# Kernel tuning notes

Measured on AMD Instinct MI355X. Metric: run time of the kernel, lower is better.

## Reference

```python
import jax, jax.numpy as jnp
import numpy as np

H = 8        # num_heads
D = 768      # d_model
DH = D // H  # d_head = 96


def setup_inputs() -> dict:
    key = jax.random.key(0)
    ks = jax.random.split(key, 12)
    B, S = 4, 2048
    s_in = 1.0 / np.sqrt(D)
    s_cat = 1.0 / np.sqrt(D)
    return {
        "input_querys": jax.random.normal(ks[0], (B, S, D), jnp.float32),
        "input_key": jax.random.normal(ks[1], (B, S, D), jnp.float32),
        "input_values": jax.random.normal(ks[2], (B, S, D), jnp.float32),
        # per-head projection weights, stacked over the head axis
        "Wq": jax.random.normal(ks[3], (H, D, DH), jnp.float32) * s_in,
        "bq": jax.random.normal(ks[4], (H, DH), jnp.float32) * s_in,
        "Wk": jax.random.normal(ks[5], (H, D, DH), jnp.float32) * s_in,
        "bk": jax.random.normal(ks[6], (H, DH), jnp.float32) * s_in,
        "Wv": jax.random.normal(ks[7], (H, D, DH), jnp.float32) * s_in,
        "bv": jax.random.normal(ks[8], (H, DH), jnp.float32) * s_in,
        # output linear: (H*DH) -> D
        "Wo": jax.random.normal(ks[9], (H * DH, D), jnp.float32) * s_cat,
        "bo": jax.random.normal(ks[10], (D,), jnp.float32) * s_cat,
    }


def reference(input_querys, input_key, input_values, Wq, bq, Wk, bk, Wv, bv, Wo, bo):
    # Per-head linear projections (vectorized over the head axis)
    # q/k/v: [B,S,D] -> [B,H,S,DH]
    Q = jnp.einsum("bsd,hdk->bhsk", input_querys, Wq) + bq[None, :, None, :]
    K = jnp.einsum("bsd,hdk->bhsk", input_key, Wk) + bk[None, :, None, :]
    V = jnp.einsum("bsd,hdk->bhsk", input_values, Wv) + bv[None, :, None, :]

    scale = 1.0 / jnp.sqrt(jnp.asarray(DH, Q.dtype))
    scores = jnp.einsum("bhsk,bhtk->bhst", Q, K) * scale  # [B,H,S,S]
    attn = jax.nn.softmax(scores, axis=-1)
    out = jnp.einsum("bhst,bhtk->bhsk", attn, V)  # [B,H,S,DH]

    # concat heads (head-major order matches torch.cat over ModuleList)
    B, _, S, _ = out.shape
    cat = out.transpose(0, 2, 1, 3).reshape(B, S, H * DH)
    return cat @ Wo + bo
```

## Files before the change

### kernel.cpp

```cpp
#include <hip/hip_runtime.h>


typedef unsigned short u16;
typedef _Float16 h16;
typedef h16 h16x8 __attribute__((ext_vector_type(8)));
typedef __fp16 fp16x2 __attribute__((ext_vector_type(2)));
typedef __fp16 fp16x4 __attribute__((ext_vector_type(4)));
typedef unsigned short u16x8 __attribute__((ext_vector_type(8)));
typedef unsigned short u16x4 __attribute__((ext_vector_type(4)));
typedef float f32x4 __attribute__((ext_vector_type(4)));

__device__ __forceinline__ u16 f2h(float f) {
  union { h16 h; u16 u; } c; c.h = (h16)f; return c.u;
}

__device__ __forceinline__ void gll16(const void* g, void* l) {
  __builtin_amdgcn_global_load_lds(
      (const __attribute__((address_space(1))) void*)g,
      (__attribute__((address_space(3))) void*)l, 16, 0, 0);
}

__global__ __launch_bounds__(256) void prep_kernel(
    const float* __restrict__ Wq, const float* __restrict__ Wk,
    const float* __restrict__ Wv, const float* __restrict__ Wo,
    const float* __restrict__ Xk, const float* __restrict__ Xv,
    const float* __restrict__ Xq,
    u16* __restrict__ WqT, u16* __restrict__ WkT,
    u16* __restrict__ WvT, u16* __restrict__ WoT,
    u16* __restrict__ Xk16, u16* __restrict__ Xv16, u16* __restrict__ Xq16)
{
  const int bid = blockIdx.x;
  const int tid = threadIdx.x;

  if (bid >= 432) {
    const int i = bid - 432;
    const int t = i / 3072;
    const long e = ((long)(i % 3072) * 256 + tid) * 8;
    const float* src = (t == 0) ? Xk : (t == 1) ? Xv : Xq;
    u16* dst = (t == 0) ? Xk16 : (t == 1) ? Xv16 : Xq16;
    f32x4 a = *(const f32x4*)(&src[e]);
    f32x4 b = *(const f32x4*)(&src[e + 4]);
    u16x8 v;
    #pragma unroll
    for (int j = 0; j < 4; j++) { v[j] = f2h(a[j]); v[4 + j] = f2h(b[j]); }
    *(u16x8*)(&dst[e]) = v;
    return;
  }

  if (bid < 288) {
    __shared__ u16 Lt[96][72];
    const int w = bid / 96;
    const int r = bid % 96;
    const int h = r / 12, dt = r % 12;
    const float* W = (w == 0) ? Wq : (w == 1) ? Wk : Wv;
    u16* T = (w == 0) ? WqT : (w == 1) ? WkT : WvT;
    const float* src = W + (size_t)h * 73728 + (size_t)dt * 64 * 96;
    #pragma unroll
    for (int p = 0; p < 6; p++) {
      const int lin = p * 1024 + tid * 4;
      f32x4 v = *(const f32x4*)(&src[lin]);
      const int d = lin / 96, kk = lin % 96;
      #pragma unroll
      for (int j = 0; j < 4; j++) Lt[kk + j][d] = f2h(v[j]);
    }
    __syncthreads();
    #pragma unroll
    for (int c = 0; c < 3; c++) {
      const int ch = c * 256 + tid;
      const int kk = ch >> 3, dc = ch & 7;
      u16x8 o = *(const u16x8*)(&Lt[kk][dc * 8]);
      *(u16x8*)(&T[(size_t)(h * 96 + kk) * 768 + dt * 64 + dc * 8]) = o;
    }
    return;
  }

  {
    __shared__ u16 Lo[64][72];
    const int i = bid - 288;
    const int kt = i / 12, nt = i % 12;
    const float* src = Wo + (size_t)(kt * 64) * 768 + nt * 64;
    #pragma unroll
    for (int p = 0; p < 4; p++) {
      const int lin = p * 1024 + tid * 4;
      const int kr = lin >> 6, nc = lin & 63;
      f32x4 v = *(const f32x4*)(&src[(size_t)kr * 768 + nc]);
      #pragma unroll
      for (int j = 0; j < 4; j++) Lo[nc + j][kr] = f2h(v[j]);
    }
    __syncthreads();
    #pragma unroll
    for (int c = 0; c < 2; c++) {
      const int ch = c * 256 + tid;
      const int nr = ch >> 3, kc = ch & 7;
      u16x8 o = *(const u16x8*)(&Lo[nr][kc * 8]);
      *(u16x8*)(&WoT[(size_t)(nt * 64 + nr) * 768 + kt * 64 + kc * 8]) = o;
    }
  }
}

#define GK 768

__global__ __launch_bounds__(256) void gemm_qkv(
    const u16* __restrict__ Xq16, const u16* __restrict__ Xk16,
    const u16* __restrict__ Xv16, const u16* __restrict__ WT,
    const float* __restrict__ bq, const float* __restrict__ bk,
    const float* __restrict__ bv,
    u16* __restrict__ Q16, u16* __restrict__ K16, u16* __restrict__ VT)
{
  const int z = blockIdx.z;
  const u16* BT = WT + (size_t)z * 589824;
  const float* bias = (z == 0) ? bq : (z == 1) ? bk : bv;
  const u16* A = (z == 0) ? Xq16 : (z == 1) ? Xk16 : Xv16;

  __shared__ __align__(16) u16 Sb[16384];

  const int tid = threadIdx.x;
  const int wave = tid >> 6;
  const int lane = tid & 63;
  const int quad = lane >> 4;
  const int l16 = lane & 15;
  const int m0 = blockIdx.x * 128;
  const int n0 = blockIdx.y * 128;

  f32x4 acc[2][8];
  #pragma unroll
  for (int i = 0; i < 2; i++)
    #pragma unroll
    for (int j = 0; j < 8; j++) acc[i][j] = (f32x4){0.f, 0.f, 0.f, 0.f};

  const int c0 = tid, c1 = tid + 256;
  const u16* gA0 = A + (size_t)(m0 + (c0 >> 2)) * GK + (c0 & 3) * 8;
  const u16* gA1 = A + (size_t)(m0 + (c1 >> 2)) * GK + (c1 & 3) * 8;
  const u16* gB0 = BT + (size_t)(n0 + (c0 >> 2)) * GK + (c0 & 3) * 8;
  const u16* gB1 = BT + (size_t)(n0 + (c1 >> 2)) * GK + (c1 & 3) * 8;
  const int ld0 = (wave * 64) * 8;
  const int ld1 = (256 + wave * 64) * 8;

#define STAGE(buf, kt) do {                                        \
    const int k0_ = (kt) * 32;                                     \
    u16* dst_ = Sb + (buf) * 8192;                                 \
    gll16(gA0 + k0_, dst_ + ld0);                                  \
    gll16(gA1 + k0_, dst_ + ld1);                                  \
    gll16(gB0 + k0_, dst_ + 4096 + ld0);                           \
    gll16(gB1 + k0_, dst_ + 4096 + ld1);                           \
  } while (0)

  STAGE(0, 0);
  int buf = 0;
  for (int kt = 0; kt < 24; kt++) {
    if (kt + 1 < 24) {
      STAGE(buf ^ 1, kt + 1);
      asm volatile("s_waitcnt vmcnt(4)" ::: "memory");
    } else {
      asm volatile("s_waitcnt vmcnt(0)" ::: "memory");
    }
    __builtin_amdgcn_s_barrier();

    const u16* As = Sb + buf * 8192;
    const u16* Bs = As + 4096;
    h16x8 af[2], bf[8];
    #pragma unroll
    for (int mf = 0; mf < 2; mf++)
      af[mf] = *(const h16x8*)(&As[(wave * 32 + mf * 16 + l16) * 32 + quad * 8]);
    #pragma unroll
    for (int nf = 0; nf < 8; nf++)
      bf[nf] = *(const h16x8*)(&Bs[(nf * 16 + l16) * 32 + quad * 8]);
    #pragma unroll
    for (int mf = 0; mf < 2; mf++)
      #pragma unroll
      for (int nf = 0; nf < 8; nf++)
        acc[mf][nf] = __builtin_amdgcn_mfma_f32_16x16x32_f16(af[mf], bf[nf], acc[mf][nf], 0, 0, 0);

    __builtin_amdgcn_s_barrier();
    buf ^= 1;
  }
#undef STAGE

  if (z == 2) {
    const int b = m0 >> 11, s0 = m0 & 2047;
    u16* Ts = Sb;
    #pragma unroll
    for (int half = 0; half < 2; half++) {
      __syncthreads();
      #pragma unroll
      for (int nf2 = 0; nf2 < 4; nf2++) {
        const int nf = half * 4 + nf2;
        const float bv2 = bias[n0 + nf * 16 + l16];
        #pragma unroll
        for (int mf = 0; mf < 2; mf++)
          #pragma unroll
          for (int r = 0; r < 4; r++)
            Ts[(nf2 * 16 + l16) * 136 + wave * 32 + mf * 16 + quad * 4 + r] =
                f2h(acc[mf][nf][r] + bv2);
      }
      __syncthreads();
      #pragma unroll
      for (int p = 0; p < 4; p++) {
        const int c = p * 256 + tid;
        const int row = c >> 4, col8 = (c & 15) * 8;
        u16x8 o8 = *(const u16x8*)(&Ts[row * 136 + col8]);
        *(u16x8*)(&VT[(size_t)b * 768 * 2048 +
                      (size_t)(n0 + half * 64 + row) * 2048 + s0 + col8]) = o8;
      }
    }
    return;
  }

  u16* Yr = (z == 0) ? Q16 : K16;
  #pragma unroll
  for (int nf = 0; nf < 8; nf++) {
    const int n = n0 + nf * 16 + l16;
    const float bv2 = bias[n];
    #pragma unroll
    for (int mf = 0; mf < 2; mf++) {
      const int m = m0 + wave * 32 + mf * 16 + quad * 4;
      #pragma unroll
      for (int r = 0; r < 4; r++)
        Yr[(size_t)(m + r) * GK + n] = f2h(acc[mf][nf][r] + bv2);
    }
  }
}

__global__ __launch_bounds__(256) void gemm_o(
    const u16* __restrict__ A, const u16* __restrict__ BT,
    const float* __restrict__ bias, float* __restrict__ Y)
{
  __shared__ __align__(16) u16 Sb[16384];

  const int tid = threadIdx.x;
  const int wave = tid >> 6;
  const int lane = tid & 63;
  const int quad = lane >> 4;
  const int l16 = lane & 15;
  const int m0 = blockIdx.x * 128;
  const int n0 = blockIdx.y * 128;

  f32x4 acc[2][8];
  #pragma unroll
  for (int i = 0; i < 2; i++)
    #pragma unroll
    for (int j = 0; j < 8; j++) acc[i][j] = (f32x4){0.f, 0.f, 0.f, 0.f};

  const int c0 = tid, c1 = tid + 256;
  const u16* gA0 = A + (size_t)(m0 + (c0 >> 2)) * GK + (c0 & 3) * 8;
  const u16* gA1 = A + (size_t)(m0 + (c1 >> 2)) * GK + (c1 & 3) * 8;
  const u16* gB0 = BT + (size_t)(n0 + (c0 >> 2)) * GK + (c0 & 3) * 8;
  const u16* gB1 = BT + (size_t)(n0 + (c1 >> 2)) * GK + (c1 & 3) * 8;
  const int ld0 = (wave * 64) * 8;
  const int ld1 = (256 + wave * 64) * 8;

#define STAGE(buf, kt) do {                                        \
    const int k0_ = (kt) * 32;                                     \
    u16* dst_ = Sb + (buf) * 8192;                                 \
    gll16(gA0 + k0_, dst_ + ld0);                                  \
    gll16(gA1 + k0_, dst_ + ld1);                                  \
    gll16(gB0 + k0_, dst_ + 4096 + ld0);                           \
    gll16(gB1 + k0_, dst_ + 4096 + ld1);                           \
  } while (0)

  STAGE(0, 0);
  int buf = 0;
  for (int kt = 0; kt < 24; kt++) {
    if (kt + 1 < 24) {
      STAGE(buf ^ 1, kt + 1);
      asm volatile("s_waitcnt vmcnt(4)" ::: "memory");
    } else {
      asm volatile("s_waitcnt vmcnt(0)" ::: "memory");
    }
    __builtin_amdgcn_s_barrier();

    const u16* As = Sb + buf * 8192;
    const u16* Bs = As + 4096;
    h16x8 af[2], bf[8];
    #pragma unroll
    for (int mf = 0; mf < 2; mf++)
      af[mf] = *(const h16x8*)(&As[(wave * 32 + mf * 16 + l16) * 32 + quad * 8]);
    #pragma unroll
    for (int nf = 0; nf < 8; nf++)
      bf[nf] = *(const h16x8*)(&Bs[(nf * 16 + l16) * 32 + quad * 8]);
    #pragma unroll
    for (int mf = 0; mf < 2; mf++)
      #pragma unroll
      for (int nf = 0; nf < 8; nf++)
        acc[mf][nf] = __builtin_amdgcn_mfma_f32_16x16x32_f16(af[mf], bf[nf], acc[mf][nf], 0, 0, 0);

    __builtin_amdgcn_s_barrier();
    buf ^= 1;
  }
#undef STAGE

  #pragma unroll
  for (int nf = 0; nf < 8; nf++) {
    const int n = n0 + nf * 16 + l16;
    const float bv = bias[n];
    #pragma unroll
    for (int mf = 0; mf < 2; mf++) {
      const int m = m0 + wave * 32 + mf * 16 + quad * 4;
      #pragma unroll
      for (int r = 0; r < 4; r++)
        Y[(size_t)(m + r) * GK + n] = acc[mf][nf][r] + bv;
    }
  }
}

#define SEQ 2048
#define NT 32
#define LQK 104
#define LVT 72
#define LPS 72

__global__ __launch_bounds__(512, 4) void attn_kernel(
    const u16* __restrict__ Q, const u16* __restrict__ K,
    const u16* __restrict__ VT, u16* __restrict__ O)
{
  __shared__ __align__(16) u16 Ks[2][64 * LQK];
  __shared__ __align__(16) u16 Vt[2][96 * LVT];
  __shared__ __align__(16) u16 Ps[8][16 * LPS];

  const int tid = threadIdx.x;
  const int wave = tid >> 6;
  const int lane = tid & 63;
  const int quad = lane >> 4;
  const int l16 = lane & 15;

  const int bh = blockIdx.y;
  const int b = bh >> 3, h = bh & 7;
  const int q0 = blockIdx.x * 128;

  const size_t batch_off = (size_t)b * SEQ * 768;
  const u16* Kg = K + batch_off + h * 96;
  const u16* Vg = VT + (size_t)b * 768 * 2048 + (size_t)(h * 96) * 2048;

  h16x8 qf[3];
  {
    const u16* Qrow = Q + batch_off + (size_t)(q0 + wave * 16 + l16) * 768 + h * 96 + quad * 8;
    #pragma unroll
    for (int ks = 0; ks < 3; ks++) qf[ks] = *(const h16x8*)(&Qrow[ks * 32]);
  }

  const int kr0 = tid / 12, kc0 = (tid % 12) * 8;
  const int kr1 = (tid + 512) / 12, kc1 = ((tid + 512) % 12) * 8;
  const int vr0 = tid >> 3, vc0 = (tid & 7) * 8;
  const int vr1 = (tid + 512) >> 3, vc1 = ((tid + 512) & 7) * 8;
  const bool extra = tid < 256;

  f32x4 o[6];
  #pragma unroll
  for (int i = 0; i < 6; i++) o[i] = (f32x4){0.f, 0.f, 0.f, 0.f};
  float m_raw = -1e30f, lrow = 0.f;
  const float sc = 0.14724498f;

  u16* Pw = &Ps[wave][0];

  u16x8 kA, kB, vA, vB;
  kA = *(const u16x8*)(&Kg[(size_t)kr0 * 768 + kc0]);
  vA = *(const u16x8*)(&Vg[(size_t)vr0 * 2048 + vc0]);
  if (extra) {
    kB = *(const u16x8*)(&Kg[(size_t)kr1 * 768 + kc1]);
    vB = *(const u16x8*)(&Vg[(size_t)vr1 * 2048 + vc1]);
  }
  *(u16x8*)(&Ks[0][kr0 * LQK + kc0]) = kA;
  *(u16x8*)(&Vt[0][vr0 * LVT + vc0]) = vA;
  if (extra) {
    *(u16x8*)(&Ks[0][kr1 * LQK + kc1]) = kB;
    *(u16x8*)(&Vt[0][vr1 * LVT + vc1]) = vB;
  }
  {
    const u16* Kn = Kg + (size_t)64 * 768;
    const u16* Vn = Vg + 64;
    kA = *(const u16x8*)(&Kn[(size_t)kr0 * 768 + kc0]);
    vA = *(const u16x8*)(&Vn[(size_t)vr0 * 2048 + vc0]);
    if (extra) {
      kB = *(const u16x8*)(&Kn[(size_t)kr1 * 768 + kc1]);
      vB = *(const u16x8*)(&Vn[(size_t)vr1 * 2048 + vc1]);
    }
  }
  __syncthreads();

  for (int kt = 0; kt < NT; kt++) {
    const int cur = kt & 1;
    const u16* Kc = &Ks[cur][0];
    const u16* Vc = &Vt[cur][0];

    f32x4 s[4];
    #pragma unroll
    for (int kf = 0; kf < 4; kf++) s[kf] = (f32x4){0.f, 0.f, 0.f, 0.f};
    __builtin_amdgcn_s_setprio(1);
    #pragma unroll
    for (int ks = 0; ks < 3; ks++) {
      #pragma unroll
      for (int kf = 0; kf < 4; kf++) {
        h16x8 a = *(const h16x8*)(&Kc[(kf * 16 + l16) * LQK + ks * 32 + quad * 8]);
        s[kf] = __builtin_amdgcn_mfma_f32_16x16x32_f16(a, qf[ks], s[kf], 0, 0, 0);
      }
    }
    __builtin_amdgcn_s_setprio(0);

    float mx = s[0][0];
    #pragma unroll
    for (int kf = 0; kf < 4; kf++)
      #pragma unroll
      for (int r = 0; r < 4; r++) mx = fmaxf(mx, s[kf][r]);
    mx = fmaxf(mx, __shfl_xor(mx, 16));
    mx = fmaxf(mx, __shfl_xor(mx, 32));
    if (__any(mx > m_raw + 54.0f)) {
      const float mnew = fmaxf(m_raw, mx);
      const float alpha = exp2f(sc * (m_raw - mnew));
      lrow *= alpha;
      #pragma unroll
      for (int nfo = 0; nfo < 6; nfo++)
        #pragma unroll
        for (int r = 0; r < 4; r++) o[nfo][r] *= alpha;
      m_raw = mnew;
    }
    const float c0f = sc * m_raw;
    float ps = 0.f;
    #pragma unroll
    for (int kf = 0; kf < 4; kf++)
      #pragma unroll
      for (int r = 0; r < 4; r++) {
        float p = exp2f(fmaf(s[kf][r], sc, -c0f));
        s[kf][r] = p;
        ps += p;
      }
    lrow += ps;

    #pragma unroll
    for (int kf = 0; kf < 4; kf++) {
      fp16x2 a2 = __builtin_amdgcn_cvt_pkrtz(s[kf][0], s[kf][1]);
      fp16x2 b2 = __builtin_amdgcn_cvt_pkrtz(s[kf][2], s[kf][3]);
      fp16x4 w4; w4[0] = a2[0]; w4[1] = a2[1]; w4[2] = b2[0]; w4[3] = b2[1];
      *(fp16x4*)(&Pw[l16 * LPS + kf * 16 + quad * 4]) = w4;
    }

    __builtin_amdgcn_s_setprio(1);
    #pragma unroll
    for (int ks = 0; ks < 2; ks++) {
      h16x8 pfr = *(const h16x8*)(&Pw[l16 * LPS + ks * 32 + quad * 8]);
      #pragma unroll
      for (int nfo = 0; nfo < 6; nfo++) {
        h16x8 vfr = *(const h16x8*)(&Vc[(nfo * 16 + l16) * LVT + ks * 32 + quad * 8]);
        o[nfo] = __builtin_amdgcn_mfma_f32_16x16x32_f16(vfr, pfr, o[nfo], 0, 0, 0);
      }
    }
    __builtin_amdgcn_s_setprio(0);

    if (kt + 1 < NT) {
      u16* Kw = &Ks[cur ^ 1][0];
      u16* Vw = &Vt[cur ^ 1][0];
      *(u16x8*)(&Kw[kr0 * LQK + kc0]) = kA;
      *(u16x8*)(&Vw[vr0 * LVT + vc0]) = vA;
      if (extra) {
        *(u16x8*)(&Kw[kr1 * LQK + kc1]) = kB;
        *(u16x8*)(&Vw[vr1 * LVT + vc1]) = vB;
      }
      if (kt + 2 < NT) {
        const u16* Kn = Kg + (size_t)(kt + 2) * 64 * 768;
        const u16* Vn = Vg + (size_t)(kt + 2) * 64;
        kA = *(const u16x8*)(&Kn[(size_t)kr0 * 768 + kc0]);
        vA = *(const u16x8*)(&Vn[(size_t)vr0 * 2048 + vc0]);
        if (extra) {
          kB = *(const u16x8*)(&Kn[(size_t)kr1 * 768 + kc1]);
          vB = *(const u16x8*)(&Vn[(size_t)vr1 * 2048 + vc1]);
        }
      }
      __syncthreads();
    }
  }

  lrow += __shfl_xor(lrow, 16);
  lrow += __shfl_xor(lrow, 32);
  const float inv = 1.0f / lrow;
  u16* Ob = O + batch_off + (size_t)(q0 + wave * 16 + l16) * 768 + h * 96;
  #pragma unroll
  for (int nfo = 0; nfo < 6; nfo++) {
    fp16x2 lo = __builtin_amdgcn_cvt_pkrtz(o[nfo][0] * inv, o[nfo][1] * inv);
    fp16x2 hi = __builtin_amdgcn_cvt_pkrtz(o[nfo][2] * inv, o[nfo][3] * inv);
    *(fp16x2*)(&Ob[nfo * 16 + quad * 4]) = lo;
    *(fp16x2*)(&Ob[nfo * 16 + quad * 4 + 2]) = hi;
  }
}

extern "C" void kernel_launch(void* const* d_in, const int* in_sizes, int n_in,
                              void* d_out, int out_size, void* d_ws, size_t ws_size,
                              hipStream_t stream) {
  const float* Xq = (const float*)d_in[0];
  const float* Xk = (const float*)d_in[1];
  const float* Xv = (const float*)d_in[2];
  const float* Wq = (const float*)d_in[3];
  const float* bq = (const float*)d_in[4];
  const float* Wk = (const float*)d_in[5];
  const float* bk = (const float*)d_in[6];
  const float* Wv = (const float*)d_in[7];
  const float* bv = (const float*)d_in[8];
  const float* Wo = (const float*)d_in[9];
  const float* bo = (const float*)d_in[10];

  u16* wsu = (u16*)d_ws;
  u16* WT   = wsu;
  u16* WoT  = wsu + 3 * 589824;
  u16* Q16  = wsu + 4 * 589824;
  u16* Xk16 = Q16 + 6291456;
  u16* Xv16 = Xk16 + 6291456;
  u16* Xq16 = Xv16 + 6291456;

  u16* outu = (u16*)d_out;
  u16* VTb = outu;
  u16* K16 = outu + 6291456;

  u16* A16 = Xk16;

  prep_kernel<<<9648, 256, 0, stream>>>(
      Wq, Wk, Wv, Wo, Xk, Xv, Xq,
      WT, WT + 589824, WT + 2 * 589824, WoT, Xk16, Xv16, Xq16);
  gemm_qkv<<<dim3(64, 6, 3), 256, 0, stream>>>(
      Xq16, Xk16, Xv16, WT, bq, bk, bv, Q16, K16, VTb);
  attn_kernel<<<dim3(16, 32), 512, 0, stream>>>(Q16, K16, VTb, A16);
  gemm_o<<<dim3(64, 6), 256, 0, stream>>>(A16, WoT, bo, (float*)d_out);
}
```

Measured before the change: 286.0 us.

## Split KV range across two wave groups with two query tiles per wave

Restructures the attention kernel so each wave handles 32 query rows (two MFMA row tiles sharing each K/V fragment read), and the two halves of the block each process half of the key sequence. A final LDS-based merge combines the partial softmax states (max, sum, output) of the two groups. The intent is to halve K/V LDS fragment reads per MFMA and keep more independent MFMAs in flight. In exchange it adds more registers per wave, a second barrier per iteration, single-buffered LDS tiles per group, and an epilogue reduction.

```diff
diff --git a/kernel.cpp b/kernel.cpp
--- a/kernel.cpp
+++ b/kernel.cpp
@@ -304,180 +304,226 @@
 }
 
 #define SEQ 2048
-#define NT 32
 #define LQK 104
 #define LVT 72
-#define LPS 72
+#define LPS 40
 
 __global__ __launch_bounds__(512, 4) void attn_kernel(
     const u16* __restrict__ Q, const u16* __restrict__ K,
     const u16* __restrict__ VT, u16* __restrict__ O)
 {
-  __shared__ __align__(16) u16 Ks[2][64 * LQK];
-  __shared__ __align__(16) u16 Vt[2][96 * LVT];
-  __shared__ __align__(16) u16 Ps[8][16 * LPS];
+  __shared__ __align__(16) u16 SMEM[13312 + 13824 + 10240];
+  u16* Ksb = SMEM;
+  u16* Vtb = SMEM + 13312;
+  u16* Psb = SMEM + 27136;
 
   const int tid = threadIdx.x;
   const int wave = tid >> 6;
   const int lane = tid & 63;
   const int quad = lane >> 4;
   const int l16 = lane & 15;
+  const int g = wave >> 2;
+  const int w4 = wave & 3;
+  const int tg = tid & 255;
 
   const int bh = blockIdx.y;
   const int b = bh >> 3, h = bh & 7;
   const int q0 = blockIdx.x * 128;
+  const int qbase = q0 + w4 * 32;
 
   const size_t batch_off = (size_t)b * SEQ * 768;
   const u16* Kg = K + batch_off + h * 96;
   const u16* Vg = VT + (size_t)b * 768 * 2048 + (size_t)(h * 96) * 2048;
 
-  h16x8 qf[3];
-  {
-    const u16* Qrow = Q + batch_off + (size_t)(q0 + wave * 16 + l16) * 768 + h * 96 + quad * 8;
-    #pragma unroll
-    for (int ks = 0; ks < 3; ks++) qf[ks] = *(const h16x8*)(&Qrow[ks * 32]);
-  }
-
-  const int kr0 = tid / 12, kc0 = (tid % 12) * 8;
-  const int kr1 = (tid + 512) / 12, kc1 = ((tid + 512) % 12) * 8;
-  const int vr0 = tid >> 3, vc0 = (tid & 7) * 8;
-  const int vr1 = (tid + 512) >> 3, vc1 = ((tid + 512) & 7) * 8;
-  const bool extra = tid < 256;
-
-  f32x4 o[6];
-  #pragma unroll
-  for (int i = 0; i < 6; i++) o[i] = (f32x4){0.f, 0.f, 0.f, 0.f};
-  float m_raw = -1e30f, lrow = 0.f;
+  h16x8 qf[2][3];
+  #pragma unroll
+  for (int mf = 0; mf < 2; mf++) {
+    const u16* Qrow = Q + batch_off +
+        (size_t)(qbase + mf * 16 + l16) * 768 + h * 96 + quad * 8;
+    #pragma unroll
+    for (int ks = 0; ks < 3; ks++) qf[mf][ks] = *(const h16x8*)(&Qrow[ks * 32]);
+  }
+
+  int kof[3], kgf[3], vof[3], vgf[3];
+  #pragma unroll
+  for (int j = 0; j < 3; j++) {
+    const int c = tg + j * 256;
+    const int kr = c / 12, kc = (c % 12) * 8;
+    const int vr = c >> 3, vc = (c & 7) * 8;
+    kof[j] = kr * LQK + kc;  kgf[j] = kr * 768 + kc;
+    vof[j] = vr * LVT + vc;  vgf[j] = vr * 2048 + vc;
+  }
+  u16* Ksg = Ksb + g * 6656;
+  u16* Vtg = Vtb + g * 6912;
+
+  f32x4 o[2][6];
+  #pragma unroll
+  for (int mf = 0; mf < 2; mf++)
+    #pragma unroll
+    for (int i = 0; i < 6; i++) o[mf][i] = (f32x4){0.f, 0.f, 0.f, 0.f};
+  float m_raw[2] = {-1e30f, -1e30f};
+  float lrow[2] = {0.f, 0.f};
   const float sc = 0.14724498f;
 
-  u16* Pw = &Ps[wave][0];
-
-  u16x8 kA, kB, vA, vB;
-  kA = *(const u16x8*)(&Kg[(size_t)kr0 * 768 + kc0]);
-  vA = *(const u16x8*)(&Vg[(size_t)vr0 * 2048 + vc0]);
-  if (extra) {
-    kB = *(const u16x8*)(&Kg[(size_t)kr1 * 768 + kc1]);
-    vB = *(const u16x8*)(&Vg[(size_t)vr1 * 2048 + vc1]);
-  }
-  *(u16x8*)(&Ks[0][kr0 * LQK + kc0]) = kA;
-  *(u16x8*)(&Vt[0][vr0 * LVT + vc0]) = vA;
-  if (extra) {
-    *(u16x8*)(&Ks[0][kr1 * LQK + kc1]) = kB;
-    *(u16x8*)(&Vt[0][vr1 * LVT + vc1]) = vB;
-  }
-  {
-    const u16* Kn = Kg + (size_t)64 * 768;
-    const u16* Vn = Vg + 64;
-    kA = *(const u16x8*)(&Kn[(size_t)kr0 * 768 + kc0]);
-    vA = *(const u16x8*)(&Vn[(size_t)vr0 * 2048 + vc0]);
-    if (extra) {
-      kB = *(const u16x8*)(&Kn[(size_t)kr1 * 768 + kc1]);
-      vB = *(const u16x8*)(&Vn[(size_t)vr1 * 2048 + vc1]);
-    }
-  }
+  u16* Pw = Psb + wave * 32 * LPS;
+
+  const int t0 = g * 16;
+  u16x8 kR[3], vR[3];
+
+#define LOADT(t) do {                                                   \
+    const u16* Kt_ = Kg + (size_t)(t) * 64 * 768;                       \
+    const u16* Vt_ = Vg + (size_t)(t) * 64;                             \
+    _Pragma("unroll")                                                   \
+    for (int j = 0; j < 3; j++) {                                       \
+      kR[j] = *(const u16x8*)(&Kt_[kgf[j]]);                            \
+      vR[j] = *(const u16x8*)(&Vt_[vgf[j]]);                            \
+    }                                                                   \
+  } while (0)
+#define WRITET() do {                                                   \
+    _Pragma("unroll")                                                   \
+    for (int j = 0; j < 3; j++) {                                       \
+      *(u16x8*)(&Ksg[kof[j]]) = kR[j];                                  \
+      *(u16x8*)(&Vtg[vof[j]]) = vR[j];                                  \
+    }                                                                   \
+  } while (0)
+
+  LOADT(t0);
+  WRITET();
+  LOADT(t0 + 1);
   __syncthreads();
 
-  for (int kt = 0; kt < NT; kt++) {
-    const int cur = kt & 1;
-    const u16* Kc = &Ks[cur][0];
-    const u16* Vc = &Vt[cur][0];
-
-    f32x4 s[4];
-    #pragma unroll
-    for (int kf = 0; kf < 4; kf++) s[kf] = (f32x4){0.f, 0.f, 0.f, 0.f};
+  for (int i = 0; i < 16; i++) {
+    f32x4 s[2][4];
+    #pragma unroll
+    for (int mf = 0; mf < 2; mf++)
+      #pragma unroll
+      for (int kf = 0; kf < 4; kf++) s[mf][kf] = (f32x4){0.f, 0.f, 0.f, 0.f};
     __builtin_amdgcn_s_setprio(1);
     #pragma unroll
     for (int ks = 0; ks < 3; ks++) {
       #pragma unroll
       for (int kf = 0; kf < 4; kf++) {
-        h16x8 a = *(const h16x8*)(&Kc[(kf * 16 + l16) * LQK + ks * 32 + quad * 8]);
-        s[kf] = __builtin_amdgcn_mfma_f32_16x16x32_f16(a, qf[ks], s[kf], 0, 0, 0);
+        h16x8 a = *(const h16x8*)(&Ksg[(kf * 16 + l16) * LQK + ks * 32 + quad * 8]);
+        s[0][kf] = __builtin_amdgcn_mfma_f32_16x16x32_f16(a, qf[0][ks], s[0][kf], 0, 0, 0);
+        s[1][kf] = __builtin_amdgcn_mfma_f32_16x16x32_f16(a, qf[1][ks], s[1][kf], 0, 0, 0);
       }
     }
     __builtin_amdgcn_s_setprio(0);
 
-    float mx = s[0][0];
-    #pragma unroll
-    for (int kf = 0; kf < 4; kf++)
-      #pragma unroll
-      for (int r = 0; r < 4; r++) mx = fmaxf(mx, s[kf][r]);
-    mx = fmaxf(mx, __shfl_xor(mx, 16));
-    mx = fmaxf(mx, __shfl_xor(mx, 32));
-    if (__any(mx > m_raw + 54.0f)) {
-      const float mnew = fmaxf(m_raw, mx);
-      const float alpha = exp2f(sc * (m_raw - mnew));
-      lrow *= alpha;
+    #pragma unroll
+    for (int mf = 0; mf < 2; mf++) {
+      float mx = s[mf][0][0];
+      #pragma unroll
+      for (int kf = 0; kf < 4; kf++)
+        #pragma unroll
+        for (int r = 0; r < 4; r++) mx = fmaxf(mx, s[mf][kf][r]);
+      mx = fmaxf(mx, __shfl_xor(mx, 16));
+      mx = fmaxf(mx, __shfl_xor(mx, 32));
+      if (__any(mx > m_raw[mf] + 54.0f)) {
+        const float mnew = fmaxf(m_raw[mf], mx);
+        const float alpha = exp2f(sc * (m_raw[mf] - mnew));
+        lrow[mf] *= alpha;
+        #pragma unroll
+        for (int nfo = 0; nfo < 6; nfo++)
+          #pragma unroll
+          for (int r = 0; r < 4; r++) o[mf][nfo][r] *= alpha;
+        m_raw[mf] = mnew;
+      }
+      const float c0 = sc * m_raw[mf];
+      float ps = 0.f;
+      #pragma unroll
+      for (int kf = 0; kf < 4; kf++)
+        #pragma unroll
+        for (int r = 0; r < 4; r++) {
+          float p = exp2f(fmaf(s[mf][kf][r], sc, -c0));
+          s[mf][kf][r] = p;
+          ps += p;
+        }
+      lrow[mf] += ps;
+    }
+
+    #pragma unroll
+    for (int hk = 0; hk < 2; hk++) {
+      #pragma unroll
+      for (int mf = 0; mf < 2; mf++)
+        #pragma unroll
+        for (int kf2 = 0; kf2 < 2; kf2++) {
+          const int kf = hk * 2 + kf2;
+          fp16x2 a2 = __builtin_amdgcn_cvt_pkrtz(s[mf][kf][0], s[mf][kf][1]);
+          fp16x2 b2 = __builtin_amdgcn_cvt_pkrtz(s[mf][kf][2], s[mf][kf][3]);
+          fp16x4 w4p; w4p[0] = a2[0]; w4p[1] = a2[1]; w4p[2] = b2[0]; w4p[3] = b2[1];
+          *(fp16x4*)(&Pw[(mf * 16 + l16) * LPS + kf2 * 16 + quad * 4]) = w4p;
+        }
+      h16x8 pf0 = *(const h16x8*)(&Pw[l16 * LPS + quad * 8]);
+      h16x8 pf1 = *(const h16x8*)(&Pw[(16 + l16) * LPS + quad * 8]);
+      __builtin_amdgcn_s_setprio(1);
+      #pragma unroll
+      for (int nfo = 0; nfo < 6; nfo++) {
+        h16x8 vfr = *(const h16x8*)(&Vtg[(nfo * 16 + l16) * LVT + hk * 32 + quad * 8]);
+        o[0][nfo] = __builtin_amdgcn_mfma_f32_16x16x32_f16(vfr, pf0, o[0][nfo], 0, 0, 0);
+        o[1][nfo] = __builtin_amdgcn_mfma_f32_16x16x32_f16(vfr, pf1, o[1][nfo], 0, 0, 0);
+      }
+      __builtin_amdgcn_s_setprio(0);
+    }
+
+    if (i + 1 < 16) {
+      __syncthreads();
+      WRITET();
+      if (i + 2 < 16) LOADT(t0 + i + 2);
+      __syncthreads();
+    }
+  }
+#undef LOADT
+#undef WRITET
+
+  __syncthreads();
+  #pragma unroll
+  for (int mf = 0; mf < 2; mf++) {
+    lrow[mf] += __shfl_xor(lrow[mf], 16);
+    lrow[mf] += __shfl_xor(lrow[mf], 32);
+  }
+  float* Ms = (float*)SMEM;
+  float* MLs = (float*)Psb;
+
+  if (g == 1) {
+    float* os = Ms + w4 * (32 * 96);
+    #pragma unroll
+    for (int mf = 0; mf < 2; mf++) {
       #pragma unroll
       for (int nfo = 0; nfo < 6; nfo++)
-        #pragma unroll
-        for (int r = 0; r < 4; r++) o[nfo][r] *= alpha;
-      m_raw = mnew;
-    }
-    const float c0f = sc * m_raw;
-    float ps = 0.f;
-    #pragma unroll
-    for (int kf = 0; kf < 4; kf++)
-      #pragma unroll
-      for (int r = 0; r < 4; r++) {
-        float p = exp2f(fmaf(s[kf][r], sc, -c0f));
-        s[kf][r] = p;
-        ps += p;
-      }
-    lrow += ps;
-
-    #pragma unroll
-    for (int kf = 0; kf < 4; kf++) {
-      fp16x2 a2 = __builtin_amdgcn_cvt_pkrtz(s[kf][0], s[kf][1]);
-      fp16x2 b2 = __builtin_amdgcn_cvt_pkrtz(s[kf][2], s[kf][3]);
-      fp16x4 w4; w4[0] = a2[0]; w4[1] = a2[1]; w4[2] = b2[0]; w4[3] = b2[1];
-      *(fp16x4*)(&Pw[l16 * LPS + kf * 16 + quad * 4]) = w4;
-    }
-
-    __builtin_amdgcn_s_setprio(1);
-    #pragma unroll
-    for (int ks = 0; ks < 2; ks++) {
-      h16x8 pfr = *(const h16x8*)(&Pw[l16 * LPS + ks * 32 + quad * 8]);
+        *(f32x4*)(&os[(mf * 16 + l16) * 96 + nfo * 16 + quad * 4]) = o[mf][nfo];
+      if (quad == 0) {
+        MLs[(w4 * 32 + mf * 16 + l16) * 2 + 0] = m_raw[mf];
+        MLs[(w4 * 32 + mf * 16 + l16) * 2 + 1] = lrow[mf];
+      }
+    }
+  }
+  __syncthreads();
+  if (g == 0) {
+    float* os = Ms + w4 * (32 * 96);
+    #pragma unroll
+    for (int mf = 0; mf < 2; mf++) {
+      const float m1 = MLs[(w4 * 32 + mf * 16 + l16) * 2 + 0];
+      const float l1 = MLs[(w4 * 32 + mf * 16 + l16) * 2 + 1];
+      const float mm = fmaxf(m_raw[mf], m1);
+      const float e0 = exp2f(sc * (m_raw[mf] - mm));
+      const float e1 = exp2f(sc * (m1 - mm));
+      const float inv = 1.0f / (e0 * lrow[mf] + e1 * l1);
+      const float a0 = e0 * inv, a1 = e1 * inv;
+      u16* Ob = O + batch_off + (size_t)(qbase + mf * 16 + l16) * 768 + h * 96;
       #pragma unroll
       for (int nfo = 0; nfo < 6; nfo++) {
-        h16x8 vfr = *(const h16x8*)(&Vc[(nfo * 16 + l16) * LVT + ks * 32 + quad * 8]);
-        o[nfo] = __builtin_amdgcn_mfma_f32_16x16x32_f16(vfr, pfr, o[nfo], 0, 0, 0);
-      }
-    }
-    __builtin_amdgcn_s_setprio(0);
-
-    if (kt + 1 < NT) {
-      u16* Kw = &Ks[cur ^ 1][0];
-      u16* Vw = &Vt[cur ^ 1][0];
-      *(u16x8*)(&Kw[kr0 * LQK + kc0]) = kA;
-      *(u16x8*)(&Vw[vr0 * LVT + vc0]) = vA;
-      if (extra) {
-        *(u16x8*)(&Kw[kr1 * LQK + kc1]) = kB;
-        *(u16x8*)(&Vw[vr1 * LVT + vc1]) = vB;
-      }
-      if (kt + 2 < NT) {
-        const u16* Kn = Kg + (size_t)(kt + 2) * 64 * 768;
-        const u16* Vn = Vg + (size_t)(kt + 2) * 64;
-        kA = *(const u16x8*)(&Kn[(size_t)kr0 * 768 + kc0]);
-        vA = *(const u16x8*)(&Vn[(size_t)vr0 * 2048 + vc0]);
-        if (extra) {
-          kB = *(const u16x8*)(&Kn[(size_t)kr1 * 768 + kc1]);
-          vB = *(const u16x8*)(&Vn[(size_t)vr1 * 2048 + vc1]);
-        }
-      }
-      __syncthreads();
-    }
-  }
-
-  lrow += __shfl_xor(lrow, 16);
-  lrow += __shfl_xor(lrow, 32);
-  const float inv = 1.0f / lrow;
-  u16* Ob = O + batch_off + (size_t)(q0 + wave * 16 + l16) * 768 + h * 96;
-  #pragma unroll
-  for (int nfo = 0; nfo < 6; nfo++) {
-    fp16x2 lo = __builtin_amdgcn_cvt_pkrtz(o[nfo][0] * inv, o[nfo][1] * inv);
-    fp16x2 hi = __builtin_amdgcn_cvt_pkrtz(o[nfo][2] * inv, o[nfo][3] * inv);
-    *(fp16x2*)(&Ob[nfo * 16 + quad * 4]) = lo;
-    *(fp16x2*)(&Ob[nfo * 16 + quad * 4 + 2]) = hi;
+        f32x4 o1 = *(const f32x4*)(&os[(mf * 16 + l16) * 96 + nfo * 16 + quad * 4]);
+        float v0 = a0 * o[mf][nfo][0] + a1 * o1[0];
+        float v1 = a0 * o[mf][nfo][1] + a1 * o1[1];
+        float v2 = a0 * o[mf][nfo][2] + a1 * o1[2];
+        float v3 = a0 * o[mf][nfo][3] + a1 * o1[3];
+        fp16x2 lo = __builtin_amdgcn_cvt_pkrtz(v0, v1);
+        fp16x2 hi = __builtin_amdgcn_cvt_pkrtz(v2, v3);
+        *(fp16x2*)(&Ob[nfo * 16 + quad * 4]) = lo;
+        *(fp16x2*)(&Ob[nfo * 16 + quad * 4 + 2]) = hi;
+      }
+    }
   }
 }
 
```

Measured after the change: 437.5 us. +53.0%, slower.
